# Kernel tuning notes

Hardware: AMD Instinct MI355X
Metric: run time of the kernel (lower is better)

The kernel has to match this reference:

```python
import jax, jax.numpy as jnp
import numpy as np

B, IN, H, K = 4096, 1024, 1024, 32  # batch, input_size, hidden_size, inner_hidden


def setup_inputs() -> dict:
    key = jax.random.key(0)
    ks = jax.random.split(key, 11)
    stdv = 1.0 / np.sqrt(H)
    u = lambda k, shp: jax.random.uniform(k, shp, jnp.float32, -stdv, stdv)
    return {
        "x": jax.random.normal(ks[0], (B, IN), jnp.float32),
        "h_prev": jax.random.normal(ks[1], (B, H), jnp.float32),
        "c_prev": jax.random.normal(ks[2], (B, H), jnp.float32),
        "Wg": u(ks[3], (3 * H, IN + H)),
        "bg": u(ks[4], (3 * H,)),
        "Wc": u(ks[5], (2 * H, IN + H)),
        "bc": u(ks[6], (2 * H,)),
        "W1": u(ks[7], (K, 2)),
        "b1": u(ks[8], (K,)),
        "W2": u(ks[9], (1, K)),
        "b2": u(ks[10], (1,)),
    }


def reference(x, h_prev, c_prev, Wg, bg, Wc, bc, W1, b1, W2, b2):
    combined = jnp.concatenate([x, h_prev], axis=1)          # [B, IN+H]
    gates = combined @ Wg.T + bg                              # [B, 3H]
    i, f, o = jnp.split(jax.nn.sigmoid(gates), 3, axis=1)     # each [B, H]
    cell_raw = combined @ Wc.T + bc                           # [B, 2H]
    pairs = cell_raw.reshape(B, H, 2)                         # [B, H, 2]
    hid = jax.nn.relu(jnp.einsum('bhp,kp->bhk', pairs, W1) + b1)  # [B, H, K]
    g = jnp.einsum('bhk,ok->bho', hid, W2)[..., 0] + b2[0]    # [B, H]
    c_next = f * c_prev + i * g
    h_next = o * jnp.tanh(c_next)
    return (h_next, c_next)
```

## Files before the change

### kernel.cpp

```cpp
#include <hip/hip_runtime.h>
#include <hip/hip_bf16.h>

#define BB   4096
#define INW  1024
#define HH   1024
#define KIN  2048
#define NG   5120
#define KH   32

typedef __bf16 bf16;
typedef __bf16 bf16x4 __attribute__((ext_vector_type(4)));
typedef __bf16 bf16x8 __attribute__((ext_vector_type(8)));
typedef float  floatx4 __attribute__((ext_vector_type(4)));

#define GLD16(gp, lp)                                                          \
  __builtin_amdgcn_global_load_lds(                                            \
      (__attribute__((address_space(1))) const void*)(gp),                     \
      (__attribute__((address_space(3))) void*)(lp), 16, 0, 0)

#define NC4  (BB * KIN / 4)
#define NWG4 (3 * HH * KIN / 4)
#define NWC4 (2 * HH * KIN / 4)

__global__ __launch_bounds__(256) void prep(
    const float* __restrict__ x, const float* __restrict__ h,
    const float* __restrict__ Wg, const float* __restrict__ Wc,
    bf16* __restrict__ comb, bf16* __restrict__ Wb) {
  int i = blockIdx.x * 256 + threadIdx.x;
  const float* src;
  bf16* dst;
  if (i < NC4) {
    int e = i * 4;
    int b = e >> 11;
    int c = e & (KIN - 1);
    src = (c < INW) ? (x + (size_t)b * INW + c) : (h + (size_t)b * HH + (c - INW));
    dst = comb + e;
  } else if (i < NC4 + NWG4) {
    int e = (i - NC4) * 4;
    src = Wg + e;
    dst = Wb + e;
  } else {
    int e = (i - NC4 - NWG4) * 4;
    src = Wc + e;
    dst = Wb + (size_t)3 * HH * KIN + e;
  }
  float4 v = *(const float4*)src;
  bf16x4 o;
  o[0] = (bf16)v.x; o[1] = (bf16)v.y; o[2] = (bf16)v.z; o[3] = (bf16)v.w;
  *(bf16x4*)dst = o;
}

__global__ __launch_bounds__(256) void gemm_bt(
    const bf16* __restrict__ A, const bf16* __restrict__ Bm,
    bf16* __restrict__ C) {
  __shared__ bf16 As[128 * 64];
  __shared__ bf16 Bs[128 * 64];

  const int tid  = threadIdx.x;
  const int wave = tid >> 6;
  const int lane = tid & 63;
  const int m0 = blockIdx.x * 128;
  const int n0 = blockIdx.y * 128;
  const int wm = (wave >> 1) * 64;
  const int wn = (wave & 1) * 64;
  const int lr = lane & 15;
  const int qd = lane >> 4;
  const int sw = lr & 7;

  floatx4 acc[4][4] = {};

  for (int kt = 0; kt < KIN / 64; ++kt) {
    const int k0 = kt * 64;
    __syncthreads();
#pragma unroll
    for (int j = 0; j < 4; ++j) {
      int q   = j * 256 + tid;
      int row = q >> 3;
      int c   = (q & 7) ^ (row & 7);
      GLD16(A + (size_t)(m0 + row) * KIN + k0 + c * 8,
            As + (size_t)(j * 256 + wave * 64) * 8);
      GLD16(Bm + (size_t)(n0 + row) * KIN + k0 + c * 8,
            Bs + (size_t)(j * 256 + wave * 64) * 8);
    }
    __syncthreads();

#pragma unroll
    for (int ks = 0; ks < 2; ++ks) {
      bf16x8 af[4], bfr[4];
#pragma unroll
      for (int mi = 0; mi < 4; ++mi)
        af[mi] = *(const bf16x8*)
            &As[(((wm + mi * 16 + lr) << 3) + ((ks * 4 + qd) ^ sw)) << 3];
#pragma unroll
      for (int ni = 0; ni < 4; ++ni)
        bfr[ni] = *(const bf16x8*)
            &Bs[(((wn + ni * 16 + lr) << 3) + ((ks * 4 + qd) ^ sw)) << 3];
#pragma unroll
      for (int mi = 0; mi < 4; ++mi)
#pragma unroll
        for (int ni = 0; ni < 4; ++ni)
          acc[mi][ni] = __builtin_amdgcn_mfma_f32_16x16x32_bf16(
              af[mi], bfr[ni], acc[mi][ni], 0, 0, 0);
    }
  }

#pragma unroll
  for (int mi = 0; mi < 4; ++mi)
#pragma unroll
    for (int ni = 0; ni < 4; ++ni) {
      size_t base = (size_t)(m0 + wm + mi * 16 + qd * 4) * NG
                    + (n0 + wn + ni * 16 + lr);
#pragma unroll
      for (int r = 0; r < 4; ++r)
        C[base + (size_t)r * NG] = (bf16)acc[mi][ni][r];
    }
}

__global__ __launch_bounds__(256) void epilogue(
    const bf16* __restrict__ G, const float* __restrict__ c_prev,
    const float* __restrict__ bg, const float* __restrict__ bc,
    const float* __restrict__ W1, const float* __restrict__ b1,
    const float* __restrict__ W2, const float* __restrict__ b2,
    float* __restrict__ h_next, float* __restrict__ c_next) {
  int idx = blockIdx.x * 256 + threadIdx.x;
  int b = idx >> 10;
  int h = idx & (HH - 1);
  const bf16* Gr = G + (size_t)b * NG;

  float gi = (float)Gr[h]          + bg[h];
  float gf = (float)Gr[HH + h]     + bg[HH + h];
  float go = (float)Gr[2 * HH + h] + bg[2 * HH + h];
  float p0 = (float)Gr[3 * HH + 2 * h]     + bc[2 * h];
  float p1 = (float)Gr[3 * HH + 2 * h + 1] + bc[2 * h + 1];

  float g = b2[0];
#pragma unroll
  for (int k = 0; k < KH; ++k) {
    float hv = fmaf(p0, W1[2 * k], fmaf(p1, W1[2 * k + 1], b1[k]));
    hv = fmaxf(hv, 0.0f);
    g = fmaf(hv, W2[k], g);
  }

  float si = 1.0f / (1.0f + __expf(-gi));
  float sf = 1.0f / (1.0f + __expf(-gf));
  float so = 1.0f / (1.0f + __expf(-go));

  float cn = sf * c_prev[idx] + si * g;
  float hn = so * tanhf(cn);
  h_next[idx] = hn;
  c_next[idx] = cn;
}

extern "C" void kernel_launch(void* const* d_in, const int* in_sizes, int n_in,
                              void* d_out, int out_size, void* d_ws, size_t ws_size,
                              hipStream_t stream) {
  const float* x      = (const float*)d_in[0];
  const float* h_prev = (const float*)d_in[1];
  const float* c_prev = (const float*)d_in[2];
  const float* Wg     = (const float*)d_in[3];
  const float* bg     = (const float*)d_in[4];
  const float* Wc     = (const float*)d_in[5];
  const float* bc     = (const float*)d_in[6];
  const float* W1     = (const float*)d_in[7];
  const float* b1     = (const float*)d_in[8];
  const float* W2     = (const float*)d_in[9];
  const float* b2     = (const float*)d_in[10];
  float* out = (float*)d_out;

  char* ws = (char*)d_ws;
  bf16* comb = (bf16*)ws;
  bf16* Wb   = (bf16*)(ws + (size_t)BB * KIN * 2);
  bf16* G    = (bf16*)(ws + (size_t)BB * KIN * 2
                          + (size_t)NG * KIN * 2);

  prep<<<(NC4 + NWG4 + NWC4) / 256, 256, 0, stream>>>(x, h_prev, Wg, Wc, comb, Wb);

  dim3 grid(BB / 128, NG / 128);
  gemm_bt<<<grid, 256, 0, stream>>>(comb, Wb, G);

  epilogue<<<(BB * HH) / 256, 256, 0, stream>>>(
      G, c_prev, bg, bc, W1, b1, W2, b2, out, out + (size_t)BB * HH);
}
```

Measured before the change: 276.9 us.

## Use 256x128 block tile with 32x32x16 MFMA in bf16 GEMM

Doubles the GEMM block tile along M to 256 rows, with each wave covering a 128x64 sub-tile, and switches from 16x16x32 to 32x32x16 bf16 MFMA instructions with 16-element accumulators. The goal is more operand reuse per LDS load and fewer MFMA issues per FLOP, which cuts LDS read traffic and global reloads of B. In exchange, LDS use and register pressure rise, and the grid halves to 16x40 = 640 blocks. That may lower occupancy and work balance across the CUs.

```diff
diff --git a/kernel.cpp b/kernel.cpp
--- a/kernel.cpp
+++ b/kernel.cpp
@@ -11,7 +11,7 @@
 typedef __bf16 bf16;
 typedef __bf16 bf16x4 __attribute__((ext_vector_type(4)));
 typedef __bf16 bf16x8 __attribute__((ext_vector_type(8)));
-typedef float  floatx4 __attribute__((ext_vector_type(4)));
+typedef float  floatx16 __attribute__((ext_vector_type(16)));
 
 #define GLD16(gp, lp)                                                          \
   __builtin_amdgcn_global_load_lds(                                            \
@@ -53,53 +53,62 @@
 __global__ __launch_bounds__(256) void gemm_bt(
     const bf16* __restrict__ A, const bf16* __restrict__ Bm,
     bf16* __restrict__ C) {
-  __shared__ bf16 As[128 * 64];
+  __shared__ bf16 As[256 * 64];
   __shared__ bf16 Bs[128 * 64];
 
   const int tid  = threadIdx.x;
   const int wave = tid >> 6;
   const int lane = tid & 63;
-  const int m0 = blockIdx.x * 128;
+  const int m0 = blockIdx.x * 256;
   const int n0 = blockIdx.y * 128;
-  const int wm = (wave >> 1) * 64;
+  const int wm = (wave >> 1) * 128;
   const int wn = (wave & 1) * 64;
-  const int lr = lane & 15;
-  const int qd = lane >> 4;
-  const int sw = lr & 7;
+  const int lr = lane & 31;
+  const int kh = lane >> 5;
 
-  floatx4 acc[4][4] = {};
+  floatx16 acc[4][2] = {};
 
   for (int kt = 0; kt < KIN / 64; ++kt) {
     const int k0 = kt * 64;
     __syncthreads();
 #pragma unroll
-    for (int j = 0; j < 4; ++j) {
+    for (int j = 0; j < 8; ++j) {
       int q   = j * 256 + tid;
       int row = q >> 3;
       int c   = (q & 7) ^ (row & 7);
       GLD16(A + (size_t)(m0 + row) * KIN + k0 + c * 8,
             As + (size_t)(j * 256 + wave * 64) * 8);
+    }
+#pragma unroll
+    for (int j = 0; j < 4; ++j) {
+      int q   = j * 256 + tid;
+      int row = q >> 3;
+      int c   = (q & 7) ^ (row & 7);
       GLD16(Bm + (size_t)(n0 + row) * KIN + k0 + c * 8,
             Bs + (size_t)(j * 256 + wave * 64) * 8);
     }
     __syncthreads();
 
 #pragma unroll
-    for (int ks = 0; ks < 2; ++ks) {
-      bf16x8 af[4], bfr[4];
+    for (int ks = 0; ks < 4; ++ks) {
+      bf16x8 af[4], bfr[2];
 #pragma unroll
-      for (int mi = 0; mi < 4; ++mi)
-        af[mi] = *(const bf16x8*)
-            &As[(((wm + mi * 16 + lr) << 3) + ((ks * 4 + qd) ^ sw)) << 3];
+      for (int mi = 0; mi < 4; ++mi) {
+        int row  = wm + mi * 32 + lr;
+        int slot = (ks * 2 + kh) ^ (row & 7);
+        af[mi] = *(const bf16x8*)&As[row * 64 + slot * 8];
+      }
 #pragma unroll
-      for (int ni = 0; ni < 4; ++ni)
-        bfr[ni] = *(const bf16x8*)
-            &Bs[(((wn + ni * 16 + lr) << 3) + ((ks * 4 + qd) ^ sw)) << 3];
+      for (int ni = 0; ni < 2; ++ni) {
+        int row  = wn + ni * 32 + lr;
+        int slot = (ks * 2 + kh) ^ (row & 7);
+        bfr[ni] = *(const bf16x8*)&Bs[row * 64 + slot * 8];
+      }
 #pragma unroll
       for (int mi = 0; mi < 4; ++mi)
 #pragma unroll
-        for (int ni = 0; ni < 4; ++ni)
-          acc[mi][ni] = __builtin_amdgcn_mfma_f32_16x16x32_bf16(
+        for (int ni = 0; ni < 2; ++ni)
+          acc[mi][ni] = __builtin_amdgcn_mfma_f32_32x32x16_bf16(
               af[mi], bfr[ni], acc[mi][ni], 0, 0, 0);
     }
   }
@@ -107,12 +116,13 @@
 #pragma unroll
   for (int mi = 0; mi < 4; ++mi)
 #pragma unroll
-    for (int ni = 0; ni < 4; ++ni) {
-      size_t base = (size_t)(m0 + wm + mi * 16 + qd * 4) * NG
-                    + (n0 + wn + ni * 16 + lr);
+    for (int ni = 0; ni < 2; ++ni) {
+      int col = n0 + wn + ni * 32 + lr;
 #pragma unroll
-      for (int r = 0; r < 4; ++r)
-        C[base + (size_t)r * NG] = (bf16)acc[mi][ni][r];
+      for (int reg = 0; reg < 16; ++reg) {
+        int row = m0 + wm + mi * 32 + (reg & 3) + 8 * (reg >> 2) + 4 * kh;
+        C[(size_t)row * NG + col] = (bf16)acc[mi][ni][reg];
+      }
     }
 }
 
@@ -175,7 +185,7 @@
 
   prep<<<(NC4 + NWG4 + NWC4) / 256, 256, 0, stream>>>(x, h_prev, Wg, Wc, comb, Wb);
 
-  dim3 grid(BB / 128, NG / 128);
+  dim3 grid(BB / 256, NG / 128);
   gemm_bt<<<grid, 256, 0, stream>>>(comb, Wb, G);
 
   epilogue<<<(BB * HH) / 256, 256, 0, stream>>>(
```

Measured after the change: 314.6 us. 1.14x slower.
